# Optimization experiments

Hardware: AMD Instinct MI355X
Metric: run time of the kernel (lower is better)

The kernel has to match this reference:

```python
import jax, jax.numpy as jnp
import numpy as np

N_PAIRS = 1_000_000
N_OBJS = 1000
X_DIM = 48


def setup_inputs() -> dict:
    key = jax.random.key(0)
    ks = jax.random.split(key, 10)
    return {
        "o1": jax.random.randint(ks[0], (N_PAIRS,), 0, N_OBJS, dtype=jnp.int64 if jax.config.jax_enable_x64 else jnp.int32),
        "o2": jax.random.randint(ks[1], (N_PAIRS,), 0, N_OBJS, dtype=jnp.int64 if jax.config.jax_enable_x64 else jnp.int32),
        "T": jax.random.normal(ks[2], (N_PAIRS, 4, 4), dtype=jnp.float32),
        "geoms": jax.random.normal(ks[3], (N_OBJS, X_DIM), dtype=jnp.float32),
        "W1": jax.random.normal(ks[4], (96, 96), dtype=jnp.float32) * 0.1,
        "b1": jax.random.normal(ks[5], (96,), dtype=jnp.float32) * 0.1,
        "W2": jax.random.normal(ks[6], (96, 96), dtype=jnp.float32) * 0.1,
        "b2": jax.random.normal(ks[7], (96,), dtype=jnp.float32) * 0.1,
        "W3": jax.random.normal(ks[8], (96, 1), dtype=jnp.float32) * 0.1,
        "b3": jax.random.normal(ks[9], (1,), dtype=jnp.float32) * 0.1,
    }


def _apply_transforms(x, T):
    # x: [N, D] treated as D//3 3-vectors; homogeneous transform by T [N,4,4].
    N, D = x.shape
    v = x.reshape(N, D // 3, 3)
    # R @ v + t  (equivalent to appending 1 and taking first 3 rows of T)
    out = jnp.einsum('nij,nxj->nxi', T[:, :3, :3], v) + T[:, :3, 3][:, None, :]
    return out.reshape(N, D)


def _mlp(x, W1, b1, W2, b2, W3, b3):
    h = jax.nn.relu(x @ W1 + b1)
    h = jax.nn.relu(h @ W2 + b2)
    return (h @ W3 + b3)[:, 0]  # squeeze -> [N]


def reference(o1, o2, T, geoms, W1, b1, W2, b2, W3, b3):
    x1 = geoms[o1]          # [N, 48]
    x2 = geoms[o2]          # [N, 48]

    def branch(a, b, Tm):
        bt = _apply_transforms(b, Tm)
        x = jnp.concatenate([a, bt], axis=1)  # [N, 96]
        return _mlp(x, W1, b1, W2, b2, W3, b3)

    d_1_2 = branch(x1, x2, T)
    T_inv = jnp.linalg.inv(T)
    d_2_1 = branch(x2, x1, T_inv)
    return 0.5 * (d_1_2 + d_2_1)
```

## Files before the change

### kernel.cpp

```cpp
#include <hip/hip_runtime.h>
#include <hip/hip_bf16.h>

typedef __attribute__((ext_vector_type(8))) short bf16x8;
typedef __attribute__((ext_vector_type(4))) float f32x4;

constexpr int BT   = 1024;
constexpr int KD   = 96;
constexpr int LDX  = 104;
constexpr int LDT  = 12;
constexpr int NBLK = 256;
constexpr int TOTW = NBLK * (BT / 64);

__device__ inline ushort f2bf(float f) {
    uint u = __float_as_uint(f);
    u += 0x7fffu + ((u >> 16) & 1u);
    return (ushort)(u >> 16);
}

__device__ inline uint f2bf2(float lo, float hi) {
    float2 t; t.x = lo; t.y = hi;
    __hip_bfloat162 h = __float22bfloat162_rn(t);
    union { __hip_bfloat162 b; uint u; } cv;
    cv.b = h;
    return cv.u;
}

__global__ void prep_geoms(const float* __restrict__ g, ushort* __restrict__ gb, int n) {
    int i = blockIdx.x * 256 + threadIdx.x;
    if (i < n) gb[i] = f2bf(g[i]);
}

__device__ inline void inv4x4(float4 t0, float4 t1, float4 t2, float4 t3,
                              float* __restrict__ ti) {
    double m00=t0.x, m01=t0.y, m02=t0.z, m03=t0.w;
    double m10=t1.x, m11=t1.y, m12=t1.z, m13=t1.w;
    double m20=t2.x, m21=t2.y, m22=t2.z, m23=t2.w;
    double m30=t3.x, m31=t3.y, m32=t3.z, m33=t3.w;
    double A2323 = m22*m33 - m23*m32;
    double A1323 = m21*m33 - m23*m31;
    double A1223 = m21*m32 - m22*m31;
    double A0323 = m20*m33 - m23*m30;
    double A0223 = m20*m32 - m22*m30;
    double A0123 = m20*m31 - m21*m30;
    double A2313 = m12*m33 - m13*m32;
    double A1313 = m11*m33 - m13*m31;
    double A1213 = m11*m32 - m12*m31;
    double A2312 = m12*m23 - m13*m22;
    double A1312 = m11*m23 - m13*m21;
    double A1212 = m11*m22 - m12*m21;
    double A0313 = m10*m33 - m13*m30;
    double A0213 = m10*m32 - m12*m30;
    double A0312 = m10*m23 - m13*m20;
    double A0212 = m10*m22 - m12*m20;
    double A0113 = m10*m31 - m11*m30;
    double A0112 = m10*m21 - m11*m20;
    double det = m00*(m11*A2323 - m12*A1323 + m13*A1223)
               - m01*(m10*A2323 - m12*A0323 + m13*A0223)
               + m02*(m10*A1323 - m11*A0323 + m13*A0123)
               - m03*(m10*A1223 - m11*A0223 + m12*A0123);
    double idet = 1.0 / det;
    ti[0]  = (float)( idet *  (m11*A2323 - m12*A1323 + m13*A1223) );
    ti[1]  = (float)( idet * -(m01*A2323 - m02*A1323 + m03*A1223) );
    ti[2]  = (float)( idet *  (m01*A2313 - m02*A1313 + m03*A1213) );
    ti[3]  = (float)( idet * -(m01*A2312 - m02*A1312 + m03*A1212) );
    ti[4]  = (float)( idet * -(m10*A2323 - m12*A0323 + m13*A0223) );
    ti[5]  = (float)( idet *  (m00*A2323 - m02*A0323 + m03*A0223) );
    ti[6]  = (float)( idet * -(m00*A2313 - m02*A0313 + m03*A0213) );
    ti[7]  = (float)( idet *  (m00*A2312 - m02*A0312 + m03*A0212) );
    ti[8]  = (float)( idet *  (m10*A1323 - m11*A0323 + m13*A0123) );
    ti[9]  = (float)( idet * -(m00*A1323 - m01*A0323 + m03*A0123) );
    ti[10] = (float)( idet *  (m00*A1313 - m01*A0313 + m03*A0113) );
    ti[11] = (float)( idet * -(m00*A1312 - m01*A0312 + m03*A0112) );
}

__global__ void __launch_bounds__(BT, 4) collision_mfma(
    const int* __restrict__ o1, const int* __restrict__ o2,
    const float* __restrict__ Tg, const float* __restrict__ geoms,
    const ushort* __restrict__ gbf,
    const float* __restrict__ W1, const float* __restrict__ b1,
    const float* __restrict__ W2, const float* __restrict__ b2,
    const float* __restrict__ W3, const float* __restrict__ b3,
    float* __restrict__ out, int N)
{
    __shared__ ushort xs[512 * LDX];
    __shared__ ushort wlds[36 * 64 * 8];
    __shared__ float  tinv[256 * LDT];
    __shared__ float  bls[292];

    const int tid = threadIdx.x;
    const int w   = tid >> 6;
    const int l   = tid & 63;
    const int cl  = l & 15;
    const int g   = l >> 4;
    const int rg  = g * 4;

    const int rl = l & 31;
    const int pt = l >> 5;
    const int br = rl >> 4;
    const int dp = rl & 15;

    for (int e = tid; e < 36 * 512; e += BT) {
        int f    = e >> 9;
        int r    = e & 511;
        int lane = r >> 3;
        int j    = r & 7;
        int L    = f / 18;
        int fr   = f - L * 18;
        int mt   = fr / 3;
        int kb   = fr - mt * 3;
        int gg   = lane >> 4;
        int cc   = lane & 15;
        const float* W = L ? W2 : W1;
        wlds[e] = f2bf(W[(kb * 32 + gg * 8 + j) * KD + mt * 16 + cc]);
    }
    if (tid < 96) {
        bls[tid]       = b1[tid];
        bls[96 + tid]  = b2[tid];
        bls[192 + tid] = W3[tid];
    }
    if (tid == 96) bls[288] = b3[0];
    __syncthreads();

    const int NWT = N >> 4;
    const int gw  = blockIdx.x * (BT / 64) + w;

    for (int wt = gw; wt < NWT; wt += TOTW) {
        const int pbase = wt * 16;

        if (l < 16) {
            const float4* T4 = reinterpret_cast<const float4*>(Tg + (size_t)(pbase + l) * 16);
            float4 t0 = T4[0], t1 = T4[1], t2 = T4[2], t3 = T4[3];
            inv4x4(t0, t1, t2, t3, &tinv[(w * 16 + l) * LDT]);
        }
        asm volatile("" ::: "memory");

        {
            const int p  = pbase + dp;
            const int ia = o1[p], ib = o2[p];
            const int oa = br ? ib : ia;
            const int ob = br ? ia : ib;
            ushort* xrow = xs + (w * 32 + rl) * LDX;

            {
                const uint4* src = reinterpret_cast<const uint4*>(gbf + oa * 48 + pt * 24);
                uint4* dst = reinterpret_cast<uint4*>(xrow + pt * 24);
                dst[0] = src[0]; dst[1] = src[1]; dst[2] = src[2];
            }

            float4 M0, M1, M2;
            if (br == 0) {
                const float4* Tp = reinterpret_cast<const float4*>(Tg + (size_t)p * 16);
                M0 = Tp[0]; M1 = Tp[1]; M2 = Tp[2];
            } else {
                const float4* t4 = reinterpret_cast<const float4*>(&tinv[(w * 16 + dp) * LDT]);
                M0 = t4[0]; M1 = t4[1]; M2 = t4[2];
            }
            float v[24];
            {
                const float4* bs = reinterpret_cast<const float4*>(geoms + (size_t)ob * 48 + pt * 24);
                #pragma unroll
                for (int q = 0; q < 6; ++q) {
                    float4 t = bs[q];
                    v[4*q+0] = t.x; v[4*q+1] = t.y; v[4*q+2] = t.z; v[4*q+3] = t.w;
                }
            }
            float o[24];
            #pragma unroll
            for (int m = 0; m < 8; ++m) {
                float vx = v[3*m+0], vy = v[3*m+1], vz = v[3*m+2];
                o[3*m+0] = fmaf(M0.x, vx, fmaf(M0.y, vy, fmaf(M0.z, vz, M0.w)));
                o[3*m+1] = fmaf(M1.x, vx, fmaf(M1.y, vy, fmaf(M1.z, vz, M1.w)));
                o[3*m+2] = fmaf(M2.x, vx, fmaf(M2.y, vy, fmaf(M2.z, vz, M2.w)));
            }
            union { uint u[12]; uint4 q4[3]; } pk;
            #pragma unroll
            for (int q = 0; q < 12; ++q)
                pk.u[q] = f2bf2(o[2*q], o[2*q+1]);
            uint4* dst = reinterpret_cast<uint4*>(xrow + 48 + pt * 24);
            dst[0] = pk.q4[0]; dst[1] = pk.q4[1]; dst[2] = pk.q4[2];
        }
        asm volatile("" ::: "memory");

        f32x4 acc[6][2];
        #pragma unroll
        for (int mt = 0; mt < 6; ++mt) {
            f32x4 bv = *reinterpret_cast<const f32x4*>(&bls[mt*16 + rg]);
            acc[mt][0] = bv;
            acc[mt][1] = bv;
        }
        bf16x8 xf[2][3];
        #pragma unroll
        for (int nt = 0; nt < 2; ++nt)
            #pragma unroll
            for (int kb = 0; kb < 3; ++kb)
                xf[nt][kb] = *reinterpret_cast<const bf16x8*>(
                    xs + (w*32 + nt*16 + cl) * LDX + kb*32 + g*8);
        #pragma unroll
        for (int mt = 0; mt < 6; ++mt) {
            bf16x8 wfr[3];
            #pragma unroll
            for (int kb = 0; kb < 3; ++kb)
                wfr[kb] = *reinterpret_cast<const bf16x8*>(
                    wlds + ((0*18 + mt*3 + kb) * 64 + l) * 8);
            #pragma unroll
            for (int nt = 0; nt < 2; ++nt)
                #pragma unroll
                for (int kb = 0; kb < 3; ++kb)
                    acc[mt][nt] = __builtin_amdgcn_mfma_f32_16x16x32_bf16(
                        wfr[kb], xf[nt][kb], acc[mt][nt], 0, 0, 0);
        }

        #pragma unroll
        for (int mt = 0; mt < 6; ++mt) {
            #pragma unroll
            for (int nt = 0; nt < 2; ++nt) {
                uint2 u2;
                u2.x = f2bf2(fmaxf(acc[mt][nt][0], 0.f), fmaxf(acc[mt][nt][1], 0.f));
                u2.y = f2bf2(fmaxf(acc[mt][nt][2], 0.f), fmaxf(acc[mt][nt][3], 0.f));
                *reinterpret_cast<uint2*>(
                    xs + (w*32 + nt*16 + cl) * LDX + mt*16 + rg) = u2;
            }
        }
        asm volatile("" ::: "memory");

        f32x4 acc2[6][2];
        #pragma unroll
        for (int mt = 0; mt < 6; ++mt) {
            f32x4 bv = *reinterpret_cast<const f32x4*>(&bls[96 + mt*16 + rg]);
            acc2[mt][0] = bv;
            acc2[mt][1] = bv;
        }
        bf16x8 hf[2][3];
        #pragma unroll
        for (int nt = 0; nt < 2; ++nt)
            #pragma unroll
            for (int kb = 0; kb < 3; ++kb)
                hf[nt][kb] = *reinterpret_cast<const bf16x8*>(
                    xs + (w*32 + nt*16 + cl) * LDX + kb*32 + g*8);
        #pragma unroll
        for (int mt = 0; mt < 6; ++mt) {
            bf16x8 wfr[3];
            #pragma unroll
            for (int kb = 0; kb < 3; ++kb)
                wfr[kb] = *reinterpret_cast<const bf16x8*>(
                    wlds + ((1*18 + mt*3 + kb) * 64 + l) * 8);
            #pragma unroll
            for (int nt = 0; nt < 2; ++nt)
                #pragma unroll
                for (int kb = 0; kb < 3; ++kb)
                    acc2[mt][nt] = __builtin_amdgcn_mfma_f32_16x16x32_bf16(
                        wfr[kb], hf[nt][kb], acc2[mt][nt], 0, 0, 0);
        }

        float pr0 = 0.f, pr1 = 0.f;
        #pragma unroll
        for (int mt = 0; mt < 6; ++mt) {
            f32x4 w3v = *reinterpret_cast<const f32x4*>(&bls[192 + mt*16 + rg]);
            pr0 = fmaf(fmaxf(acc2[mt][0][0], 0.f), w3v[0], pr0);
            pr0 = fmaf(fmaxf(acc2[mt][0][1], 0.f), w3v[1], pr0);
            pr0 = fmaf(fmaxf(acc2[mt][0][2], 0.f), w3v[2], pr0);
            pr0 = fmaf(fmaxf(acc2[mt][0][3], 0.f), w3v[3], pr0);
            pr1 = fmaf(fmaxf(acc2[mt][1][0], 0.f), w3v[0], pr1);
            pr1 = fmaf(fmaxf(acc2[mt][1][1], 0.f), w3v[1], pr1);
            pr1 = fmaf(fmaxf(acc2[mt][1][2], 0.f), w3v[2], pr1);
            pr1 = fmaf(fmaxf(acc2[mt][1][3], 0.f), w3v[3], pr1);
        }
        pr0 += __shfl_xor(pr0, 16, 64);
        pr0 += __shfl_xor(pr0, 32, 64);
        pr1 += __shfl_xor(pr1, 16, 64);
        pr1 += __shfl_xor(pr1, 32, 64);
        if (l < 16)
            out[pbase + l] = 0.5f * (pr0 + pr1) + bls[288];

        asm volatile("" ::: "memory");
    }
}

extern "C" void kernel_launch(void* const* d_in, const int* in_sizes, int n_in,
                              void* d_out, int out_size, void* d_ws, size_t ws_size,
                              hipStream_t stream) {
    const int*   o1    = (const int*)d_in[0];
    const int*   o2    = (const int*)d_in[1];
    const float* T     = (const float*)d_in[2];
    const float* geoms = (const float*)d_in[3];
    const float* W1    = (const float*)d_in[4];
    const float* b1    = (const float*)d_in[5];
    const float* W2    = (const float*)d_in[6];
    const float* b2    = (const float*)d_in[7];
    const float* W3    = (const float*)d_in[8];
    const float* b3    = (const float*)d_in[9];
    float* out = (float*)d_out;
    const int N  = in_sizes[0];
    const int NG = in_sizes[3];

    ushort* gbf = (ushort*)d_ws;
    hipLaunchKernelGGL(prep_geoms, dim3((NG + 255) / 256), dim3(256), 0, stream,
                       geoms, gbf, NG);
    hipLaunchKernelGGL(collision_mfma, dim3(NBLK), dim3(BT), 0, stream,
                       o1, o2, T, geoms, gbf, W1, b1, W2, b2, W3, b3, out, N);
}
```

Baseline: 134.4 us.

## Precompute 4x4 inverses in a separate kernel and drop per-tile LDS staging

Adds a prep_tinv kernel that inverts every T matrix into a workspace buffer when the workspace is large enough. The main kernel then reads the inverse rows straight from global memory instead of having 16 lanes per wave invert in double precision and stage through LDS. It also removes the compiler memory barriers and routes weight and bias LDS reads through an opaque offset so address arithmetic is not rematerialised. The trade-off is an extra pass that reads all of T and writes 48 MB of inverses, plus an extra kernel launch. Removing the barriers relies on intra-wave ordering of the LDS accesses.

```diff
diff --git a/kernel.cpp b/kernel.cpp
--- a/kernel.cpp
+++ b/kernel.cpp
@@ -10,6 +10,8 @@
 constexpr int LDT  = 12;
 constexpr int NBLK = 256;
 constexpr int TOTW = NBLK * (BT / 64);
+
+constexpr size_t GBF_BYTES = 48000 * 2;
 
 __device__ inline ushort f2bf(float f) {
     uint u = __float_as_uint(f);
@@ -73,10 +75,25 @@
     ti[11] = (float)( idet * -(m00*A1312 - m01*A0312 + m03*A0112) );
 }
 
+__global__ void __launch_bounds__(256) prep_tinv(const float* __restrict__ Tg,
+                                                 float* __restrict__ tg, int N) {
+    int i = blockIdx.x * 256 + threadIdx.x;
+    if (i >= N) return;
+    const float4* T4 = reinterpret_cast<const float4*>(Tg + (size_t)i * 16);
+    float4 t0 = T4[0], t1 = T4[1], t2 = T4[2], t3 = T4[3];
+    float ti[12];
+    inv4x4(t0, t1, t2, t3, ti);
+    float4* dst = reinterpret_cast<float4*>(tg + (size_t)i * 12);
+    dst[0] = *reinterpret_cast<float4*>(&ti[0]);
+    dst[1] = *reinterpret_cast<float4*>(&ti[4]);
+    dst[2] = *reinterpret_cast<float4*>(&ti[8]);
+}
+
+template<int PREINV>
 __global__ void __launch_bounds__(BT, 4) collision_mfma(
     const int* __restrict__ o1, const int* __restrict__ o2,
     const float* __restrict__ Tg, const float* __restrict__ geoms,
-    const ushort* __restrict__ gbf,
+    const ushort* __restrict__ gbf, const float* __restrict__ tinvg,
     const float* __restrict__ W1, const float* __restrict__ b1,
     const float* __restrict__ W2, const float* __restrict__ b2,
     const float* __restrict__ W3, const float* __restrict__ b3,
@@ -84,8 +101,8 @@
 {
     __shared__ ushort xs[512 * LDX];
     __shared__ ushort wlds[36 * 64 * 8];
-    __shared__ float  tinv[256 * LDT];
     __shared__ float  bls[292];
+    __shared__ float  tinv[PREINV ? 4 : 256 * LDT];
 
     const int tid = threadIdx.x;
     const int w   = tid >> 6;
@@ -127,12 +144,18 @@
     for (int wt = gw; wt < NWT; wt += TOTW) {
         const int pbase = wt * 16;
 
-        if (l < 16) {
-            const float4* T4 = reinterpret_cast<const float4*>(Tg + (size_t)(pbase + l) * 16);
-            float4 t0 = T4[0], t1 = T4[1], t2 = T4[2], t3 = T4[3];
-            inv4x4(t0, t1, t2, t3, &tinv[(w * 16 + l) * LDT]);
-        }
-        asm volatile("" ::: "memory");
+        uint off0 = 0;
+        asm volatile("" : "+v"(off0));
+        const ushort* wp = wlds + off0;
+        const float*  bp = bls + off0;
+
+        if constexpr (!PREINV) {
+            if (l < 16) {
+                const float4* T4 = reinterpret_cast<const float4*>(Tg + (size_t)(pbase + l) * 16);
+                float4 t0 = T4[0], t1 = T4[1], t2 = T4[2], t3 = T4[3];
+                inv4x4(t0, t1, t2, t3, &tinv[(w * 16 + l) * LDT]);
+            }
+        }
 
         {
             const int p  = pbase + dp;
@@ -152,8 +175,13 @@
                 const float4* Tp = reinterpret_cast<const float4*>(Tg + (size_t)p * 16);
                 M0 = Tp[0]; M1 = Tp[1]; M2 = Tp[2];
             } else {
-                const float4* t4 = reinterpret_cast<const float4*>(&tinv[(w * 16 + dp) * LDT]);
-                M0 = t4[0]; M1 = t4[1]; M2 = t4[2];
+                if constexpr (PREINV) {
+                    const float4* t4 = reinterpret_cast<const float4*>(tinvg + (size_t)p * 12);
+                    M0 = t4[0]; M1 = t4[1]; M2 = t4[2];
+                } else {
+                    const float4* t4 = reinterpret_cast<const float4*>(&tinv[(w * 16 + dp) * LDT]);
+                    M0 = t4[0]; M1 = t4[1]; M2 = t4[2];
+                }
             }
             float v[24];
             {
@@ -179,12 +207,11 @@
             uint4* dst = reinterpret_cast<uint4*>(xrow + 48 + pt * 24);
             dst[0] = pk.q4[0]; dst[1] = pk.q4[1]; dst[2] = pk.q4[2];
         }
-        asm volatile("" ::: "memory");
 
         f32x4 acc[6][2];
         #pragma unroll
         for (int mt = 0; mt < 6; ++mt) {
-            f32x4 bv = *reinterpret_cast<const f32x4*>(&bls[mt*16 + rg]);
+            f32x4 bv = *reinterpret_cast<const f32x4*>(bp + mt*16 + rg);
             acc[mt][0] = bv;
             acc[mt][1] = bv;
         }
@@ -201,7 +228,7 @@
             #pragma unroll
             for (int kb = 0; kb < 3; ++kb)
                 wfr[kb] = *reinterpret_cast<const bf16x8*>(
-                    wlds + ((0*18 + mt*3 + kb) * 64 + l) * 8);
+                    wp + ((0*18 + mt*3 + kb) * 64 + l) * 8);
             #pragma unroll
             for (int nt = 0; nt < 2; ++nt)
                 #pragma unroll
@@ -221,12 +248,11 @@
                     xs + (w*32 + nt*16 + cl) * LDX + mt*16 + rg) = u2;
             }
         }
-        asm volatile("" ::: "memory");
 
         f32x4 acc2[6][2];
         #pragma unroll
         for (int mt = 0; mt < 6; ++mt) {
-            f32x4 bv = *reinterpret_cast<const f32x4*>(&bls[96 + mt*16 + rg]);
+            f32x4 bv = *reinterpret_cast<const f32x4*>(bp + 96 + mt*16 + rg);
             acc2[mt][0] = bv;
             acc2[mt][1] = bv;
         }
@@ -243,7 +269,7 @@
             #pragma unroll
             for (int kb = 0; kb < 3; ++kb)
                 wfr[kb] = *reinterpret_cast<const bf16x8*>(
-                    wlds + ((1*18 + mt*3 + kb) * 64 + l) * 8);
+                    wp + ((1*18 + mt*3 + kb) * 64 + l) * 8);
             #pragma unroll
             for (int nt = 0; nt < 2; ++nt)
                 #pragma unroll
@@ -255,7 +281,7 @@
         float pr0 = 0.f, pr1 = 0.f;
         #pragma unroll
         for (int mt = 0; mt < 6; ++mt) {
-            f32x4 w3v = *reinterpret_cast<const f32x4*>(&bls[192 + mt*16 + rg]);
+            f32x4 w3v = *reinterpret_cast<const f32x4*>(bp + 192 + mt*16 + rg);
             pr0 = fmaf(fmaxf(acc2[mt][0][0], 0.f), w3v[0], pr0);
             pr0 = fmaf(fmaxf(acc2[mt][0][1], 0.f), w3v[1], pr0);
             pr0 = fmaf(fmaxf(acc2[mt][0][2], 0.f), w3v[2], pr0);
@@ -270,9 +296,7 @@
         pr1 += __shfl_xor(pr1, 16, 64);
         pr1 += __shfl_xor(pr1, 32, 64);
         if (l < 16)
-            out[pbase + l] = 0.5f * (pr0 + pr1) + bls[288];
-
-        asm volatile("" ::: "memory");
+            out[pbase + l] = 0.5f * (pr0 + pr1) + bp[288];
     }
 }
 
@@ -293,9 +317,21 @@
     const int N  = in_sizes[0];
     const int NG = in_sizes[3];
 
-    ushort* gbf = (ushort*)d_ws;
+    ushort* gbf   = (ushort*)d_ws;
+    float*  tinvg = (float*)((char*)d_ws + GBF_BYTES);
+    const bool pre = ws_size >= GBF_BYTES + (size_t)N * 12 * sizeof(float);
+
     hipLaunchKernelGGL(prep_geoms, dim3((NG + 255) / 256), dim3(256), 0, stream,
                        geoms, gbf, NG);
-    hipLaunchKernelGGL(collision_mfma, dim3(NBLK), dim3(BT), 0, stream,
-                       o1, o2, T, geoms, gbf, W1, b1, W2, b2, W3, b3, out, N);
-}
+    if (pre) {
+        hipLaunchKernelGGL(prep_tinv, dim3((N + 255) / 256), dim3(256), 0, stream,
+                           T, tinvg, N);
+        hipLaunchKernelGGL((collision_mfma<1>), dim3(NBLK), dim3(BT), 0, stream,
+                           o1, o2, T, geoms, gbf, tinvg,
+                           W1, b1, W2, b2, W3, b3, out, N);
+    } else {
+        hipLaunchKernelGGL((collision_mfma<0>), dim3(NBLK), dim3(BT), 0, stream,
+                           o1, o2, T, geoms, gbf, (const float*)nullptr,
+                           W1, b1, W2, b2, W3, b3, out, N);
+    }
+}
```

After: 143.2 us. 6.5% more time.
